# Kernel tuning notes

Hardware: AMD Instinct MI355X
Metric: run time of the kernel (lower is better)

## Reference

```python
import jax, jax.numpy as jnp
import numpy as np

N_EMB = 1024
HEAD_SIZE = 64
BLOCK_SIZE = 2048
B, T = 8, 2048


def setup_inputs() -> dict:
    key = jax.random.key(0)
    kx, kq, kk, kv = jax.random.split(key, 4)
    scale = 1.0 / (N_EMB ** 0.5)
    x = jax.random.normal(kx, (B, T, N_EMB), dtype=jnp.float32)
    Wq = jax.random.uniform(kq, (N_EMB, HEAD_SIZE), dtype=jnp.float32) * scale
    Wk = jax.random.uniform(kk, (N_EMB, HEAD_SIZE), dtype=jnp.float32) * scale
    Wv = jax.random.uniform(kv, (N_EMB, HEAD_SIZE), dtype=jnp.float32) * scale
    return {"x": x, "Wq": Wq, "Wk": Wk, "Wv": Wv}


def reference(x, Wq, Wk, Wv):
    # Faithful to Head.__call__ with is_training=False.
    # NOTE: original code applies NO 1/sqrt(head_size) scaling to the scores.
    Bt, Tt, _ = x.shape
    q = x @ Wq                      # (B, T, H)
    k = x @ Wk                      # (B, T, H)
    v = x @ Wv                      # (B, T, H)
    wei = jnp.einsum('bth,bsh->bts', q, k)  # (B, T, T)
    causal = jnp.tril(jnp.ones((Tt, Tt), dtype=bool))
    wei = jnp.where(causal, wei, -jnp.inf)
    wei = jax.nn.softmax(wei, axis=-1)
    out = jnp.einsum('bts,bsh->bth', wei, v)  # (B, T, H)
    return out
```

## Files before the change

kernel.cpp:

```cpp
#include <hip/hip_runtime.h>
#include <hip/hip_bf16.h>

#define BB 8
#define TT 2048
#define EE 1024
#define HH 64

typedef __attribute__((ext_vector_type(8))) short short8;
typedef __attribute__((ext_vector_type(4))) float f32x4;

__device__ inline f32x4 mfma_16x16x32(short8 a, short8 b, f32x4 c) {
  return __builtin_amdgcn_mfma_f32_16x16x32_bf16(a, b, c, 0, 0, 0);
}

__device__ inline void gload_lds16(const __hip_bfloat16* g, __hip_bfloat16* l) {
  __builtin_amdgcn_global_load_lds((const __attribute__((address_space(1))) void*)g,
                                   (__attribute__((address_space(3))) void*)l,
                                   16, 0, 0);
}

__device__ inline short f2bf(float f) {
  __hip_bfloat16 h = __float2bfloat16(f);
  return *reinterpret_cast<short*>(&h);
}
__device__ inline float bf2f(short s) {
  __hip_bfloat16 h = *reinterpret_cast<__hip_bfloat16*>(&s);
  return __bfloat162float(h);
}

#define WAIT_LGKM0() __builtin_amdgcn_s_waitcnt(0xC07F)
#define SCHED_FENCE() __builtin_amdgcn_sched_barrier(0)
#define ASM_WAIT_VM4()  asm volatile("s_waitcnt vmcnt(4)" ::: "memory")
#define ASM_WAIT_VM0()  asm volatile("s_waitcnt vmcnt(0)" ::: "memory")

__global__ void prep_w(const float* __restrict__ Wq, const float* __restrict__ Wk,
                       const float* __restrict__ Wv,
                       __hip_bfloat16* __restrict__ Wthi,
                       __hip_bfloat16* __restrict__ Wtlo,
                       float* __restrict__ maxk2) {
  const int n = blockIdx.x;
  if (n == 0 && threadIdx.x < 8) maxk2[threadIdx.x] = 0.f;
  const int m = n >> 6;
  const int h = n & 63;
  const float* W = (m == 0) ? Wq : (m == 1) ? Wk : Wv;
  const int e0 = threadIdx.x * 4;
#pragma unroll
  for (int j = 0; j < 4; ++j) {
    const float w = W[(e0 + j) * 64 + h];
    const __hip_bfloat16 hi = __float2bfloat16(w);
    Wthi[n * 1024 + e0 + j] = hi;
    Wtlo[n * 1024 + e0 + j] = __float2bfloat16(w - __bfloat162float(hi));
  }
}

__global__ __launch_bounds__(256) void qkv_gemm(
    const float* __restrict__ x,
    const __hip_bfloat16* __restrict__ Wthi, const __hip_bfloat16* __restrict__ Wtlo,
    __hip_bfloat16* __restrict__ qhi, __hip_bfloat16* __restrict__ qlo,
    __hip_bfloat16* __restrict__ khi, __hip_bfloat16* __restrict__ klo,
    __hip_bfloat16* __restrict__ vT, float* __restrict__ maxk2) {
  __shared__ __hip_bfloat16 Bsm[2][320 * 64];
  float* Ksm = (float*)&Bsm[0][0];

  const int tid  = threadIdx.x;
  const int wave = tid >> 6;
  const int lane = tid & 63;
  const int row0 = blockIdx.x * 64;
  const int l15 = lane & 15, l4 = lane >> 4;

  const float* xA = x + (size_t)(row0 + wave * 16 + l15) * 1024 + l4 * 8;

  f32x4 acc[12];
#pragma unroll
  for (int j = 0; j < 12; ++j) acc[j] = f32x4{0.f, 0.f, 0.f, 0.f};

  auto issue_B = [&](int c, int buf) {
    const int g = (lane & 7) ^ ((lane >> 3) & 7);
#pragma unroll
    for (int s = 0; s < 6; ++s) {
      const int qq = wave * 6 + s;
      const int n  = qq * 8 + (lane >> 3);
      gload_lds16(Wthi + n * 1024 + c * 64 + g * 8, &Bsm[buf][qq * 512]);
      if (qq < 16)
        gload_lds16(Wtlo + n * 1024 + c * 64 + g * 8, &Bsm[buf][192 * 64 + qq * 512]);
    }
  };
  auto load_x = [&](int c, f32x4* sl) {
    const f32x4* p0 = (const f32x4*)(xA + c * 64);
    const f32x4* p1 = (const f32x4*)(xA + c * 64 + 32);
    sl[0] = p0[0]; sl[1] = p0[1]; sl[2] = p1[0]; sl[3] = p1[1];
  };
  auto convert_A = [&](const f32x4* sp, short8& ah0, short8& ah1,
                       short8& al0, short8& al1) {
    const float* xf = (const float*)sp;
#pragma unroll
    for (int i = 0; i < 8; ++i) {
      const float v = xf[i];
      const short h = f2bf(v);
      ah0[i] = h;
      al0[i] = f2bf(v - bf2f(h));
    }
#pragma unroll
    for (int i = 0; i < 8; ++i) {
      const float v = xf[8 + i];
      const short h = f2bf(v);
      ah1[i] = h;
      al1[i] = f2bf(v - bf2f(h));
    }
  };
  auto compute = [&](int buf, const short8& ah0, const short8& ah1,
                     const short8& al0, const short8& al1) {
    const __hip_bfloat16* Bh = &Bsm[buf][0];
    const __hip_bfloat16* Bl = &Bsm[buf][192 * 64];
#pragma unroll
    for (int j = 0; j < 12; ++j) {
      const int n  = j * 16 + l15;
      const int o0 = ((l4)     ^ (n & 7)) * 8;
      const int o1 = ((4 + l4) ^ (n & 7)) * 8;
      short8 bh0 = *(const short8*)&Bh[n * 64 + o0];
      short8 bh1 = *(const short8*)&Bh[n * 64 + o1];
      acc[j] = mfma_16x16x32(ah0, bh0, acc[j]);
      acc[j] = mfma_16x16x32(ah1, bh1, acc[j]);
      if (j < 8) {
        short8 bl0 = *(const short8*)&Bl[n * 64 + o0];
        short8 bl1 = *(const short8*)&Bl[n * 64 + o1];
        acc[j] = mfma_16x16x32(ah0, bl0, acc[j]);
        acc[j] = mfma_16x16x32(ah1, bl1, acc[j]);
        acc[j] = mfma_16x16x32(al0, bh0, acc[j]);
        acc[j] = mfma_16x16x32(al1, bh1, acc[j]);
      }
    }
  };

  f32x4 xs0[4], xs1[4];
  load_x(0, xs0);
  issue_B(0, 0);
  load_x(1, xs1);
  ASM_WAIT_VM4();
  SCHED_FENCE();
  __builtin_amdgcn_s_barrier();
  SCHED_FENCE();

#pragma unroll
  for (int c = 0; c < 16; ++c) {
    const int p = c & 1;
    short8 ah0, ah1, al0, al1;
    convert_A((p == 0) ? xs0 : xs1, ah0, ah1, al0, al1);
    if (c < 15) issue_B(c + 1, p ^ 1);
    if (c < 14) load_x(c + 2, (p == 0) ? xs0 : xs1);
    SCHED_FENCE();
    compute(p, ah0, ah1, al0, al1);
    if (c < 15) {
      if (c < 14) { ASM_WAIT_VM4(); }
      else        { ASM_WAIT_VM0(); }
      SCHED_FENCE();
      __builtin_amdgcn_s_barrier();
      SCHED_FENCE();
    }
  }

  const int strip = wave * 16;
#pragma unroll
  for (int j = 0; j < 12; ++j) {
    const int n  = j * 16 + l15;
    const int mm = n >> 6;
    const int h  = n & 63;
#pragma unroll
    for (int r = 0; r < 4; ++r) {
      const int trow = row0 + strip + l4 * 4 + r;
      const float val = acc[j][r];
      const __hip_bfloat16 hi = __float2bfloat16(val);
      const __hip_bfloat16 lo = __float2bfloat16(val - __bfloat162float(hi));
      if (mm == 0) {
        qhi[trow * 64 + h] = hi;
        qlo[trow * 64 + h] = lo;
      } else if (mm == 1) {
        khi[trow * 64 + h] = hi;
        klo[trow * 64 + h] = lo;
      } else {
        const int bb = trow >> 11, tl = trow & 2047;
        vT[(bb * 64 + h) * 2048 + tl] = hi;
      }
    }
  }

#pragma unroll
  for (int r = 0; r < 4; ++r) {
    float s2 = acc[4][r] * acc[4][r] + acc[5][r] * acc[5][r] +
               acc[6][r] * acc[6][r] + acc[7][r] * acc[7][r];
    s2 += __shfl_xor(s2, 1);
    s2 += __shfl_xor(s2, 2);
    s2 += __shfl_xor(s2, 4);
    s2 += __shfl_xor(s2, 8);
    if (l15 == 0) Ksm[wave * 16 + l4 * 4 + r] = s2;
  }
  __syncthreads();
  if (wave == 0) {
    float k2 = Ksm[lane];
#pragma unroll
    for (int off = 1; off < 64; off <<= 1) k2 = fmaxf(k2, __shfl_xor(k2, off));
    if (lane == 0)
      atomicMax((int*)&maxk2[row0 >> 11], __float_as_int(k2));
  }
}

__global__ __launch_bounds__(256, 2) void attn(
    const __hip_bfloat16* __restrict__ qhi, const __hip_bfloat16* __restrict__ qlo,
    const __hip_bfloat16* __restrict__ khi, const __hip_bfloat16* __restrict__ klo,
    const __hip_bfloat16* __restrict__ vT, const float* __restrict__ maxk2,
    float* __restrict__ out) {
  __shared__ __hip_bfloat16 Psm[4][2][16 * 72];
  __shared__ float Osm[4][32][65];
  __shared__ float Lsm[4][32];

  const int tid  = threadIdx.x;
  const int wave = tid >> 6;
  const int lane = tid & 63;
  const int l15 = lane & 15, l4 = lane >> 4;

  const int b = blockIdx.x & 7;
  const int g = blockIdx.x >> 3;
  const int ss = (g < 32) ? (63 - g) : (g - 32);
  const int t0 = ss * 32;
  const int ntiles = (ss >> 1) + 1;

  short8 qh0[2], qh1[2], ql0[2], ql1[2];
#pragma unroll
  for (int m = 0; m < 2; ++m) {
    const __hip_bfloat16* qph = qhi + (b * 2048 + t0 + m * 16 + l15) * 64;
    const __hip_bfloat16* qpl = qlo + (b * 2048 + t0 + m * 16 + l15) * 64;
    qh0[m] = *(const short8*)(qph + l4 * 8);
    qh1[m] = *(const short8*)(qph + 32 + l4 * 8);
    ql0[m] = *(const short8*)(qpl + l4 * 8);
    ql1[m] = *(const short8*)(qpl + 32 + l4 * 8);
  }

  const float kmax = sqrtf(maxk2[b]);
  float c_[2][4];
#pragma unroll
  for (int m = 0; m < 2; ++m) {
    float qn = 0.f;
#pragma unroll
    for (int i = 0; i < 8; ++i) {
      const float v0 = bf2f(qh0[m][i]) + bf2f(ql0[m][i]);
      const float v1 = bf2f(qh1[m][i]) + bf2f(ql1[m][i]);
      qn += v0 * v0 + v1 * v1;
    }
    qn += __shfl_xor(qn, 16);
    qn += __shfl_xor(qn, 32);
    const float crow = sqrtf(qn) * kmax + 2.0f;
#pragma unroll
    for (int r = 0; r < 4; ++r) c_[m][r] = __shfl(crow, l4 * 4 + r);
  }

  short8 ones;
#pragma unroll
  for (int i = 0; i < 8; ++i) ones[i] = (short)0x3F80;

  f32x4 acc[2][4];
#pragma unroll
  for (int m = 0; m < 2; ++m)
#pragma unroll
    for (int j = 0; j < 4; ++j) acc[m][j] = f32x4{0.f, 0.f, 0.f, 0.f};
  f32x4 accL[2];
  accL[0] = f32x4{0.f, 0.f, 0.f, 0.f};
  accL[1] = f32x4{0.f, 0.f, 0.f, 0.f};

  const __hip_bfloat16* kbase_h = khi + (size_t)b * 2048 * 64;
  const __hip_bfloat16* kbase_l = klo + (size_t)b * 2048 * 64;
  const __hip_bfloat16* vbase   = vT + (size_t)b * 64 * 2048;

  short8 kh0[4], kh1[4], kl0[4], kl1[4];
  auto load_K = [&](int k0) {
#pragma unroll
    for (int j = 0; j < 4; ++j) {
      const __hip_bfloat16* kph = kbase_h + (k0 + j * 16 + l15) * 64;
      const __hip_bfloat16* kpl = kbase_l + (k0 + j * 16 + l15) * 64;
      kh0[j] = *(const short8*)(kph + l4 * 8);
      kh1[j] = *(const short8*)(kph + 32 + l4 * 8);
      kl0[j] = *(const short8*)(kpl + l4 * 8);
      kl1[j] = *(const short8*)(kpl + 32 + l4 * 8);
    }
  };

  if (wave < ntiles) load_K(wave << 6);

  for (int kt = wave; kt < ntiles; kt += 4) {
    const int k0 = kt << 6;
    const bool diag = (kt == ntiles - 1);

    f32x4 s_[4];
#pragma unroll
    for (int m = 0; m < 2; ++m) {
      const int rowmax = t0 + m * 16 + 15;
#pragma unroll
      for (int j = 0; j < 4; ++j) {
        if (diag && (k0 + j * 16) > rowmax) {
          s_[j] = f32x4{-1e30f, -1e30f, -1e30f, -1e30f};
        } else {
          f32x4 z = f32x4{0.f, 0.f, 0.f, 0.f};
          z = mfma_16x16x32(qh0[m], kh0[j], z);
          z = mfma_16x16x32(qh1[m], kh1[j], z);
          z = mfma_16x16x32(qh0[m], kl0[j], z);
          z = mfma_16x16x32(qh1[m], kl1[j], z);
          z = mfma_16x16x32(ql0[m], kh0[j], z);
          z = mfma_16x16x32(ql1[m], kh1[j], z);
          s_[j] = z;
        }
      }
      if (m == 1) break;
      if (diag) {
#pragma unroll
        for (int j = 0; j < 4; ++j) {
          const int key = k0 + j * 16 + l15;
#pragma unroll
          for (int r = 0; r < 4; ++r)
            if (key > (t0 + l4 * 4 + r)) s_[j][r] = -1e30f;
        }
      }
#pragma unroll
      for (int j = 0; j < 4; ++j)
#pragma unroll
        for (int r = 0; r < 4; ++r) {
          const float pv = __expf(s_[j][r] - c_[0][r]);
          Psm[wave][0][(l4 * 4 + r) * 72 + j * 16 + l15] = __float2bfloat16(pv);
        }
    }

    short8 vf0[4], vf1[4];
#pragma unroll
    for (int j = 0; j < 4; ++j) {
      const __hip_bfloat16* vp = vbase + (j * 16 + l15) * 2048 + k0;
      vf0[j] = *(const short8*)(vp + l4 * 8);
      vf1[j] = *(const short8*)(vp + 32 + l4 * 8);
    }
    if (kt + 4 < ntiles) load_K((kt + 4) << 6);

    if (diag) {
#pragma unroll
      for (int j = 0; j < 4; ++j) {
        const int key = k0 + j * 16 + l15;
#pragma unroll
        for (int r = 0; r < 4; ++r)
          if (key > (t0 + 16 + l4 * 4 + r)) s_[j][r] = -1e30f;
      }
    }
#pragma unroll
    for (int j = 0; j < 4; ++j)
#pragma unroll
      for (int r = 0; r < 4; ++r) {
        const float pv = __expf(s_[j][r] - c_[1][r]);
        Psm[wave][1][(l4 * 4 + r) * 72 + j * 16 + l15] = __float2bfloat16(pv);
      }

    WAIT_LGKM0();

#pragma unroll
    for (int m = 0; m < 2; ++m) {
      const short8 pf0 = *(const short8*)&Psm[wave][m][l15 * 72 + l4 * 8];
      const short8 pf1 = *(const short8*)&Psm[wave][m][l15 * 72 + 32 + l4 * 8];
#pragma unroll
      for (int j = 0; j < 4; ++j) {
        acc[m][j] = mfma_16x16x32(pf0, vf0[j], acc[m][j]);
        acc[m][j] = mfma_16x16x32(pf1, vf1[j], acc[m][j]);
      }
      accL[m] = mfma_16x16x32(pf0, ones, accL[m]);
      accL[m] = mfma_16x16x32(pf1, ones, accL[m]);
    }
  }

#pragma unroll
  for (int m = 0; m < 2; ++m) {
#pragma unroll
    for (int j = 0; j < 4; ++j)
#pragma unroll
      for (int r = 0; r < 4; ++r)
        Osm[wave][m * 16 + l4 * 4 + r][j * 16 + l15] = acc[m][j][r];
    if (l15 == 0) {
#pragma unroll
      for (int r = 0; r < 4; ++r)
        Lsm[wave][m * 16 + l4 * 4 + r] = accL[m][r];
    }
  }
  __syncthreads();

#pragma unroll
  for (int rr = 0; rr < 8; ++rr) {
    const int row = wave * 8 + rr;
    const float L = Lsm[0][row] + Lsm[1][row] + Lsm[2][row] + Lsm[3][row];
    const float O = Osm[0][row][lane] + Osm[1][row][lane] +
                    Osm[2][row][lane] + Osm[3][row][lane];
    out[(b * 2048 + t0 + row) * 64 + lane] = O / L;
  }
}

extern "C" void kernel_launch(void* const* d_in, const int* in_sizes, int n_in,
                              void* d_out, int out_size, void* d_ws, size_t ws_size,
                              hipStream_t stream) {
  const float* x  = (const float*)d_in[0];
  const float* Wq = (const float*)d_in[1];
  const float* Wk = (const float*)d_in[2];
  const float* Wv = (const float*)d_in[3];
  float* out = (float*)d_out;

  char* ws = (char*)d_ws;
  __hip_bfloat16* Wthi = (__hip_bfloat16*)ws;
  __hip_bfloat16* Wtlo = (__hip_bfloat16*)(ws + 393216);
  __hip_bfloat16* qhi  = (__hip_bfloat16*)(ws + 786432);
  __hip_bfloat16* qlo  = (__hip_bfloat16*)(ws + 786432 + 1 * 2097152);
  __hip_bfloat16* khi  = (__hip_bfloat16*)(ws + 786432 + 2 * 2097152);
  __hip_bfloat16* klo  = (__hip_bfloat16*)(ws + 786432 + 3 * 2097152);
  __hip_bfloat16* vT   = (__hip_bfloat16*)(ws + 786432 + 4 * 2097152);
  float* maxk2         = (float*)(ws + 786432 + 5 * 2097152);

  prep_w<<<192, 256, 0, stream>>>(Wq, Wk, Wv, Wthi, Wtlo, maxk2);
  qkv_gemm<<<256, 256, 0, stream>>>(x, Wthi, Wtlo, qhi, qlo, khi, klo, vT, maxk2);
  attn<<<512, 256, 0, stream>>>(qhi, qlo, khi, klo, vT, maxk2, out);
}
```

Before: 148.6 us.

## Halve QKV GEMM row tile and split N columns across wave pairs

The QKV projection block now covers 32 rows instead of 64. Each pair of waves shares a 16-row strip and splits the 12 output column tiles between them by parity, so the grid doubles to 512 blocks and per-wave accumulators drop from 12 to 6. The aim is to fill more CUs on the MI355X and cut register pressure. In exchange, each block reloads the full W tile into LDS for half as many rows, which doubles W traffic per row. The K-norm reduction is rewritten to sum partial squared norms from the two waves that share a row.

```diff
diff --git a/kernel.cpp b/kernel.cpp
--- a/kernel.cpp
+++ b/kernel.cpp
@@ -65,14 +65,16 @@
   const int tid  = threadIdx.x;
   const int wave = tid >> 6;
   const int lane = tid & 63;
-  const int row0 = blockIdx.x * 64;
+  const int row0 = blockIdx.x * 32;
   const int l15 = lane & 15, l4 = lane >> 4;
-
-  const float* xA = x + (size_t)(row0 + wave * 16 + l15) * 1024 + l4 * 8;
-
-  f32x4 acc[12];
-#pragma unroll
-  for (int j = 0; j < 12; ++j) acc[j] = f32x4{0.f, 0.f, 0.f, 0.f};
+  const int mhalf = wave & 1;
+  const int jpar  = wave >> 1;
+
+  const float* xA = x + (size_t)(row0 + mhalf * 16 + l15) * 1024 + l4 * 8;
+
+  f32x4 acc[6];
+#pragma unroll
+  for (int t = 0; t < 6; ++t) acc[t] = f32x4{0.f, 0.f, 0.f, 0.f};
 
   auto issue_B = [&](int c, int buf) {
     const int g = (lane & 7) ^ ((lane >> 3) & 7);
@@ -113,21 +115,22 @@
     const __hip_bfloat16* Bh = &Bsm[buf][0];
     const __hip_bfloat16* Bl = &Bsm[buf][192 * 64];
 #pragma unroll
-    for (int j = 0; j < 12; ++j) {
+    for (int t = 0; t < 6; ++t) {
+      const int j  = jpar + 2 * t;
       const int n  = j * 16 + l15;
       const int o0 = ((l4)     ^ (n & 7)) * 8;
       const int o1 = ((4 + l4) ^ (n & 7)) * 8;
       short8 bh0 = *(const short8*)&Bh[n * 64 + o0];
       short8 bh1 = *(const short8*)&Bh[n * 64 + o1];
-      acc[j] = mfma_16x16x32(ah0, bh0, acc[j]);
-      acc[j] = mfma_16x16x32(ah1, bh1, acc[j]);
-      if (j < 8) {
+      acc[t] = mfma_16x16x32(ah0, bh0, acc[t]);
+      acc[t] = mfma_16x16x32(ah1, bh1, acc[t]);
+      if (t < 4) {
         short8 bl0 = *(const short8*)&Bl[n * 64 + o0];
         short8 bl1 = *(const short8*)&Bl[n * 64 + o1];
-        acc[j] = mfma_16x16x32(ah0, bl0, acc[j]);
-        acc[j] = mfma_16x16x32(ah1, bl1, acc[j]);
-        acc[j] = mfma_16x16x32(al0, bh0, acc[j]);
-        acc[j] = mfma_16x16x32(al1, bh1, acc[j]);
+        acc[t] = mfma_16x16x32(ah0, bl0, acc[t]);
+        acc[t] = mfma_16x16x32(ah1, bl1, acc[t]);
+        acc[t] = mfma_16x16x32(al0, bh0, acc[t]);
+        acc[t] = mfma_16x16x32(al1, bh1, acc[t]);
       }
     }
   };
@@ -159,16 +162,16 @@
     }
   }
 
-  const int strip = wave * 16;
-#pragma unroll
-  for (int j = 0; j < 12; ++j) {
+#pragma unroll
+  for (int t = 0; t < 6; ++t) {
+    const int j  = jpar + 2 * t;
     const int n  = j * 16 + l15;
     const int mm = n >> 6;
     const int h  = n & 63;
 #pragma unroll
     for (int r = 0; r < 4; ++r) {
-      const int trow = row0 + strip + l4 * 4 + r;
-      const float val = acc[j][r];
+      const int trow = row0 + mhalf * 16 + l4 * 4 + r;
+      const float val = acc[t][r];
       const __hip_bfloat16 hi = __float2bfloat16(val);
       const __hip_bfloat16 lo = __float2bfloat16(val - __bfloat162float(hi));
       if (mm == 0) {
@@ -186,8 +189,7 @@
 
 #pragma unroll
   for (int r = 0; r < 4; ++r) {
-    float s2 = acc[4][r] * acc[4][r] + acc[5][r] * acc[5][r] +
-               acc[6][r] * acc[6][r] + acc[7][r] * acc[7][r];
+    float s2 = acc[2][r] * acc[2][r] + acc[3][r] * acc[3][r];
     s2 += __shfl_xor(s2, 1);
     s2 += __shfl_xor(s2, 2);
     s2 += __shfl_xor(s2, 4);
@@ -196,7 +198,9 @@
   }
   __syncthreads();
   if (wave == 0) {
-    float k2 = Ksm[lane];
+    const int ri = lane & 31;
+    const int hf = ri >> 4, rw = ri & 15;
+    float k2 = Ksm[hf * 16 + rw] + Ksm[(2 + hf) * 16 + rw];
 #pragma unroll
     for (int off = 1; off < 64; off <<= 1) k2 = fmaxf(k2, __shfl_xor(k2, off));
     if (lane == 0)
@@ -414,6 +418,6 @@
   float* maxk2         = (float*)(ws + 786432 + 5 * 2097152);
 
   prep_w<<<192, 256, 0, stream>>>(Wq, Wk, Wv, Wthi, Wtlo, maxk2);
-  qkv_gemm<<<256, 256, 0, stream>>>(x, Wthi, Wtlo, qhi, qlo, khi, klo, vT, maxk2);
+  qkv_gemm<<<512, 256, 0, stream>>>(x, Wthi, Wtlo, qhi, qlo, khi, klo, vT, maxk2);
   attn<<<512, 256, 0, stream>>>(qhi, qlo, khi, klo, vT, maxk2, out);
 }
```

New measurement: 155.5 us. +4.6%, slower.
